# Performance work log

Hardware: AMD Instinct MI355X
Metric: run time of the kernel (lower is better)

The kernel has to match this reference:

```python
import jax, jax.numpy as jnp
import numpy as np
import math

L = 6        # num_layers
H = 16       # nhead
D = 1024     # feature_dim (= d_model, dim_factor=1)
DFF = 1024
IN = 1024    # input_dim
B, T = 16, 512
HD = D // H
EPS = 1e-5


def _get_slopes(n):
    def pow2(n):
        start = 2.0 ** (-2.0 ** (-(math.log2(n) - 3)))
        return [start * (start ** i) for i in range(n)]
    if math.log2(n).is_integer():
        return pow2(n)
    cp2 = 2 ** math.floor(math.log2(n))
    return pow2(cp2) + _get_slopes(2 * cp2)[0::2][: n - cp2]


def _alibi_bias(num_heads, seq_len):
    # init_alibi_biased_mask_future reduces to -slope_h * |i - j|
    slopes = jnp.asarray(_get_slopes(num_heads), dtype=jnp.float32)  # [H]
    idx = jnp.arange(seq_len)
    rel = -jnp.abs(idx[:, None] - idx[None, :]).astype(jnp.float32)  # [T,T]
    return slopes[:, None, None] * rel  # [H,T,T]


def _ln(x, w, b):
    m = jnp.mean(x, axis=-1, keepdims=True)
    v = jnp.mean(jnp.square(x - m), axis=-1, keepdims=True)
    return (x - m) * jax.lax.rsqrt(v + EPS) * w + b


def setup_inputs() -> dict:
    key = jax.random.key(0)
    ks = jax.random.split(key, 16)
    s = 0.02
    return {
        "x": jax.random.normal(ks[0], (B, T, IN), dtype=jnp.float32),
        "bn_w": jax.random.normal(ks[1], (D, IN), dtype=jnp.float32) * s,
        "bn_b": jnp.zeros((D,), jnp.float32),
        "qkv_w": jax.random.normal(ks[2], (L, 3 * D, D), dtype=jnp.float32) * s,
        "qkv_b": jnp.zeros((L, 3 * D), jnp.float32),
        "out_w": jax.random.normal(ks[3], (L, D, D), dtype=jnp.float32) * s,
        "out_b": jnp.zeros((L, D), jnp.float32),
        "ln1_w": jnp.ones((L, D), jnp.float32),
        "ln1_b": jnp.zeros((L, D), jnp.float32),
        "ln2_w": jnp.ones((L, D), jnp.float32),
        "ln2_b": jnp.zeros((L, D), jnp.float32),
        "ff1_w": jax.random.normal(ks[4], (L, DFF, D), dtype=jnp.float32) * s,
        "ff1_b": jnp.zeros((L, DFF), jnp.float32),
        "ff2_w": jax.random.normal(ks[5], (L, D, DFF), dtype=jnp.float32) * s,
        "ff2_b": jnp.zeros((L, D), jnp.float32),
    }


def reference(x, bn_w, bn_b, qkv_w, qkv_b, out_w, out_b,
              ln1_w, ln1_b, ln2_w, ln2_b, ff1_w, ff1_b, ff2_w, ff2_b):
    b, t, _ = x.shape
    bias = _alibi_bias(H, t)  # [H,T,T], same for all batch elements
    h = x @ bn_w.T + bn_b  # bottleneck -> [B,T,D]
    scale = 1.0 / math.sqrt(HD)
    for l in range(L):
        qkv = h @ qkv_w[l].T + qkv_b[l]  # [B,T,3D]
        q, k, v = jnp.split(qkv, 3, axis=-1)
        q = q.reshape(b, t, H, HD)
        k = k.reshape(b, t, H, HD)
        v = v.reshape(b, t, H, HD)
        scores = jnp.einsum('bihd,bjhd->bhij', q, k) * scale + bias[None]
        attn = jax.nn.softmax(scores, axis=-1)
        o = jnp.einsum('bhij,bjhd->bihd', attn, v).reshape(b, t, D)
        o = o @ out_w[l].T + out_b[l]
        h = _ln(h + o, ln1_w[l], ln1_b[l])  # post-norm (PyTorch default)
        f = jax.nn.gelu(h @ ff1_w[l].T + ff1_b[l], approximate=False)
        f = f @ ff2_w[l].T + ff2_b[l]
        h = _ln(h + f, ln2_w[l], ln2_b[l])
    return h
```

## Files before the change

### kernel.cpp

```cpp
#include <hip/hip_runtime.h>
#include <stdint.h>

#define DEV static __device__ __forceinline__

typedef __attribute__((ext_vector_type(8))) uint16_t u16x8;
typedef __attribute__((ext_vector_type(4))) uint16_t u16x4;
typedef __attribute__((ext_vector_type(4))) float    f32x4;
typedef __attribute__((ext_vector_type(8))) __bf16   bf16x8;

typedef __attribute__((address_space(3))) void lds_void;
typedef __attribute__((address_space(1))) void gbl_void;

DEV float bf2f(uint16_t u){
  union { uint32_t i; float f; } v; v.i = ((uint32_t)u) << 16; return v.f;
}
DEV uint16_t f2bf(float f){ return __builtin_bit_cast(uint16_t, (__bf16)f); }
DEV f32x4 mfma16(u16x8 a, u16x8 b, f32x4 c){
  return __builtin_amdgcn_mfma_f32_16x16x32_bf16(
      __builtin_bit_cast(bf16x8, a), __builtin_bit_cast(bf16x8, b), c, 0, 0, 0);
}

__global__ __launch_bounds__(256)
void te_cvt(const float* __restrict__ in, uint16_t* __restrict__ out)
{
  const size_t i = ((size_t)blockIdx.x * 256 + threadIdx.x) * 8;
  f32x4 a = *(const f32x4*)(in + i);
  f32x4 b = *(const f32x4*)(in + i + 4);
  u16x8 o;
#pragma unroll
  for (int e = 0; e < 4; e++) {
    o[e]     = f2bf(a[e]);
    o[e + 4] = f2bf(b[e]);
  }
  *(u16x8*)(out + i) = o;
}

template<int MODE>
__global__ __launch_bounds__(256)
void te_gemm_bb(const uint16_t* __restrict__ A, int lda,
                const uint16_t* __restrict__ W, const float* __restrict__ bias,
                uint16_t* __restrict__ outB, float* __restrict__ outF,
                int M, int N, int K)
{
  __shared__ uint16_t la[128 * 64];
  __shared__ uint16_t lb[128 * 64];
  const int tid = threadIdx.x;
  const int w = tid >> 6, l = tid & 63;
  const int lr = l & 15, lg = l >> 4;
  const int tm = blockIdx.y * 128, tn = blockIdx.x * 128;
  const int srow = l >> 3;
  const int scol = ((l & 7) ^ srow) * 8;
  const int wr = (w >> 1) * 64, wc = (w & 1) * 64;

  f32x4 acc[4][4] = {};

  for (int k0 = 0; k0 < K; k0 += 64) {
#pragma unroll
    for (int c = 0; c < 4; c++) {
      const int rb = (c * 4 + w) * 8;
      const uint16_t* ga = A + (size_t)(tm + rb + srow) * lda + (k0 + scol);
      __builtin_amdgcn_global_load_lds((gbl_void*)(uintptr_t)ga,
                                       (lds_void*)(la + rb * 64), 16, 0, 0);
      const uint16_t* gw = W + (size_t)(tn + rb + srow) * K + (k0 + scol);
      __builtin_amdgcn_global_load_lds((gbl_void*)(uintptr_t)gw,
                                       (lds_void*)(lb + rb * 64), 16, 0, 0);
    }
    __syncthreads();
#pragma unroll
    for (int kk = 0; kk < 2; kk++) {
      u16x8 af[4], bfr[4];
#pragma unroll
      for (int i = 0; i < 4; i++) {
        const int row = wr + i * 16 + lr;
        af[i] = *(const u16x8*)&la[row * 64 + (((kk * 4 + lg) ^ (lr & 7)) << 3)];
      }
#pragma unroll
      for (int j = 0; j < 4; j++) {
        const int row = wc + j * 16 + lr;
        bfr[j] = *(const u16x8*)&lb[row * 64 + (((kk * 4 + lg) ^ (lr & 7)) << 3)];
      }
#pragma unroll
      for (int i = 0; i < 4; i++)
#pragma unroll
        for (int j = 0; j < 4; j++)
          acc[i][j] = mfma16(af[i], bfr[j], acc[i][j]);
    }
    __syncthreads();
  }

  float bv[4];
#pragma unroll
  for (int j = 0; j < 4; j++) bv[j] = bias[tn + wc + j * 16 + lr];
#pragma unroll
  for (int i = 0; i < 4; i++)
#pragma unroll
    for (int j = 0; j < 4; j++)
#pragma unroll
      for (int r = 0; r < 4; r++) {
        const int row = tm + wr + i * 16 + lg * 4 + r;
        const int col = tn + wc + j * 16 + lr;
        float v = acc[i][j][r] + bv[j];
        if (MODE == 2) {
          const float u = 0.7978845608028654f * v * (1.0f + 0.044715f * v * v);
          const float t = 1.0f - 2.0f / (__expf(2.0f * u) + 1.0f);
          v = 0.5f * v * (1.0f + t);
        }
        const size_t idx = (size_t)row * N + col;
        outB[idx] = f2bf(v);
        if (MODE == 1) outF[idx] = v;
      }
}

__global__ __launch_bounds__(256)
void te_attn(uint16_t* __restrict__ qkv)
{
  __shared__ uint16_t kl[64 * 64];
  __shared__ uint16_t vt[64 * 64];
  __shared__ uint16_t pl[4 * 16 * 64];
  const int tid = threadIdx.x;
  const int w = tid >> 6, l = tid & 63;
  const int lr = l & 15, lg = l >> 4;
  const int bh = blockIdx.x;
  const int qt = blockIdx.y;
  const int h  = bh & 15;
  const int b  = bh >> 4;

  u16x8 qf[2];
  {
    const size_t qoff = ((size_t)(b * 512 + qt * 64 + w * 16 + lr)) * 3072 + h * 64 + lg * 8;
    qf[0] = *(const u16x8*)&qkv[qoff];
    qf[1] = *(const u16x8*)&qkv[qoff + 32];
  }
  const float slope = exp2f(-0.5f * (float)(h + 1));
  const float scale = 0.125f;
  const int iBase = qt * 64 + w * 16 + lg * 4;

  float m[4], sd[4];
  f32x4 acc[4] = {};
#pragma unroll
  for (int r = 0; r < 4; r++) { m[r] = -1e30f; sd[r] = 0.0f; }

  for (int jt = 0; jt < 512; jt += 64) {
#pragma unroll
    for (int cc = 0; cc < 2; cc++) {
      const int c = tid + cc * 256;
      const int j = c >> 3, d0 = (c & 7) * 8;
      const size_t rbase = ((size_t)(b * 512 + jt + j)) * 3072 + h * 64 + d0;
      u16x8 kv = *(const u16x8*)&qkv[rbase + 1024];
      *(u16x8*)&kl[j * 64 + (((d0 >> 3) ^ (j & 7)) << 3)] = kv;
      u16x8 vv = *(const u16x8*)&qkv[rbase + 2048];
      const int cV = (((j >> 3) ^ (d0 >> 3)) << 3) + (j & 7);
#pragma unroll
      for (int e = 0; e < 8; e++) vt[(d0 + e) * 64 + cV] = vv[e];
    }
    __syncthreads();

    f32x4 s[4] = {};
#pragma unroll
    for (int kk = 0; kk < 2; kk++) {
#pragma unroll
      for (int n = 0; n < 4; n++) {
        const int row = n * 16 + lr;
        u16x8 kf = *(const u16x8*)&kl[row * 64 + (((kk * 4 + lg) ^ (lr & 7)) << 3)];
        s[n] = mfma16(qf[kk], kf, s[n]);
      }
    }
    float mt[4] = { -1e30f, -1e30f, -1e30f, -1e30f };
#pragma unroll
    for (int n = 0; n < 4; n++)
#pragma unroll
      for (int r = 0; r < 4; r++) {
        const int dj = (iBase + r) - (jt + n * 16 + lr);
        const float v = s[n][r] * scale - slope * fabsf((float)dj);
        s[n][r] = v;
        mt[r] = fmaxf(mt[r], v);
      }
#pragma unroll
    for (int r = 0; r < 4; r++)
#pragma unroll
      for (int msk = 1; msk < 16; msk <<= 1)
        mt[r] = fmaxf(mt[r], __shfl_xor(mt[r], msk, 16));
    float fac[4], rsum[4];
#pragma unroll
    for (int r = 0; r < 4; r++) {
      const float mn = fmaxf(m[r], mt[r]);
      fac[r] = __expf(m[r] - mn);
      m[r] = mn;
      rsum[r] = 0.0f;
    }
#pragma unroll
    for (int n = 0; n < 4; n++)
#pragma unroll
      for (int r = 0; r < 4; r++) {
        const float p = __expf(s[n][r] - m[r]);
        s[n][r] = p;
        rsum[r] += p;
      }
#pragma unroll
    for (int r = 0; r < 4; r++) {
#pragma unroll
      for (int msk = 1; msk < 16; msk <<= 1)
        rsum[r] += __shfl_xor(rsum[r], msk, 16);
      sd[r] = sd[r] * fac[r] + rsum[r];
    }
#pragma unroll
    for (int n = 0; n < 4; n++)
#pragma unroll
      for (int r = 0; r < 4; r++) acc[n][r] *= fac[r];

#pragma unroll
    for (int n = 0; n < 4; n++)
#pragma unroll
      for (int r = 0; r < 4; r++) {
        const int q = lg * 4 + r;
        const int chunk = ((2 * n + (lr >> 3)) ^ (q & 7)) & 7;
        pl[w * 1024 + q * 64 + chunk * 8 + (lr & 7)] = f2bf(s[n][r]);
      }

#pragma unroll
    for (int kk = 0; kk < 2; kk++) {
      u16x8 pf = *(const u16x8*)&pl[w * 1024 + lr * 64 + (((kk * 4 + lg) ^ (lr & 7)) << 3)];
#pragma unroll
      for (int n = 0; n < 4; n++) {
        const int row = n * 16 + lr;
        u16x8 vf = *(const u16x8*)&vt[row * 64 + ((((kk * 4 + lg) ^ (2 * n + (lr >> 3))) & 7) << 3)];
        acc[n] = mfma16(pf, vf, acc[n]);
      }
    }
    __syncthreads();
  }

#pragma unroll
  for (int n = 0; n < 4; n++)
#pragma unroll
    for (int r = 0; r < 4; r++) {
      const int i = iBase + r;
      const int d = h * 64 + n * 16 + lr;
      qkv[((size_t)(b * 512 + i)) * 3072 + d] = f2bf(acc[n][r] / sd[r]);
    }
}

template<int FINAL>
__global__ __launch_bounds__(256)
void te_ln(const float* __restrict__ hres, const uint16_t* __restrict__ delta,
           const float* __restrict__ w, const float* __restrict__ b,
           float* __restrict__ hout, uint16_t* __restrict__ bout)
{
  const int row = blockIdx.x, t = threadIdx.x;
  const size_t base = (size_t)row * 1024 + t * 4;
  f32x4 hv = *(const f32x4*)&hres[base];
  u16x4 dv = *(const u16x4*)&delta[base];
  float x[4];
#pragma unroll
  for (int i = 0; i < 4; i++) x[i] = hv[i] + bf2f(dv[i]);
  float s = x[0] + x[1] + x[2] + x[3];
  float ss = x[0]*x[0] + x[1]*x[1] + x[2]*x[2] + x[3]*x[3];
#pragma unroll
  for (int msk = 32; msk >= 1; msk >>= 1) {
    s  += __shfl_xor(s, msk);
    ss += __shfl_xor(ss, msk);
  }
  __shared__ float rs[4], rq[4];
  const int wv = t >> 6;
  if ((t & 63) == 0) { rs[wv] = s; rq[wv] = ss; }
  __syncthreads();
  s  = rs[0] + rs[1] + rs[2] + rs[3];
  ss = rq[0] + rq[1] + rq[2] + rq[3];
  const float mean = s * (1.0f / 1024.0f);
  const float var  = ss * (1.0f / 1024.0f) - mean * mean;
  const float rstd = rsqrtf(var + 1e-5f);
  f32x4 wv4 = *(const f32x4*)&w[t * 4];
  f32x4 bv4 = *(const f32x4*)&b[t * 4];
  f32x4 yo; u16x4 bo;
#pragma unroll
  for (int i = 0; i < 4; i++) {
    const float y = (x[i] - mean) * rstd * wv4[i] + bv4[i];
    yo[i] = y; bo[i] = f2bf(y);
  }
  *(f32x4*)&hout[base] = yo;
  if (FINAL == 0) *(u16x4*)&bout[base] = bo;
}

extern "C" void kernel_launch(void* const* d_in, const int* in_sizes, int n_in,
                              void* d_out, int out_size, void* d_ws, size_t ws_size,
                              hipStream_t stream)
{
  (void)in_sizes; (void)n_in; (void)out_size; (void)ws_size;
  const float* x     = (const float*)d_in[0];
  const float* bn_w  = (const float*)d_in[1];
  const float* bn_b  = (const float*)d_in[2];
  const float* qkv_w = (const float*)d_in[3];
  const float* qkv_b = (const float*)d_in[4];
  const float* out_w = (const float*)d_in[5];
  const float* out_b = (const float*)d_in[6];
  const float* ln1_w = (const float*)d_in[7];
  const float* ln1_b = (const float*)d_in[8];
  const float* ln2_w = (const float*)d_in[9];
  const float* ln2_b = (const float*)d_in[10];
  const float* ff1_w = (const float*)d_in[11];
  const float* ff1_b = (const float*)d_in[12];
  const float* ff2_w = (const float*)d_in[13];
  const float* ff2_b = (const float*)d_in[14];

  char* ws = (char*)d_ws;
  float*    h_f32   = (float*)ws;
  uint16_t* h_bf    = (uint16_t*)(ws + (32u  << 20));
  uint16_t* qkvb    = (uint16_t*)(ws + (48u  << 20));
  uint16_t* scrA    = (uint16_t*)(ws + (96u  << 20));
  uint16_t* qkvw_bf = (uint16_t*)(ws + (112u << 20));
  uint16_t* ff2w_bf = (uint16_t*)(ws + (148u << 20));
  uint16_t* bnw_bf  = (uint16_t*)(ws + (160u << 20));
  uint16_t* outw_bf = (uint16_t*)d_out;
  uint16_t* ff1w_bf = (uint16_t*)((char*)d_out + (12u << 20));
  float*    outf    = (float*)d_out;

  const int M = 8192;
  dim3 blk(256);

  te_cvt<<<dim3(18874368 / 2048), blk, 0, stream>>>(qkv_w, qkvw_bf);
  te_cvt<<<dim3(6291456  / 2048), blk, 0, stream>>>(out_w, outw_bf);
  te_cvt<<<dim3(6291456  / 2048), blk, 0, stream>>>(ff1_w, ff1w_bf);
  te_cvt<<<dim3(6291456  / 2048), blk, 0, stream>>>(ff2_w, ff2w_bf);
  te_cvt<<<dim3(1048576  / 2048), blk, 0, stream>>>(bn_w,  bnw_bf);
  te_cvt<<<dim3(8388608  / 2048), blk, 0, stream>>>(x,     scrA);

  te_gemm_bb<1><<<dim3(8, 64), blk, 0, stream>>>(scrA, 1024, bnw_bf, bn_b,
                                                 h_bf, h_f32, M, 1024, 1024);

  for (int l = 0; l < 6; l++) {
    te_gemm_bb<0><<<dim3(24, 64), blk, 0, stream>>>(
        h_bf, 1024, qkvw_bf + (size_t)l * 3072 * 1024, qkv_b + l * 3072,
        qkvb, nullptr, M, 3072, 1024);
    te_attn<<<dim3(256, 8), blk, 0, stream>>>(qkvb);
    te_gemm_bb<0><<<dim3(8, 64), blk, 0, stream>>>(
        qkvb, 3072, outw_bf + (size_t)l * 1024 * 1024, out_b + l * 1024,
        scrA, nullptr, M, 1024, 1024);
    te_ln<0><<<dim3(8192), blk, 0, stream>>>(h_f32, scrA, ln1_w + l * 1024, ln1_b + l * 1024,
                                             h_f32, h_bf);
    te_gemm_bb<2><<<dim3(8, 64), blk, 0, stream>>>(
        h_bf, 1024, ff1w_bf + (size_t)l * 1024 * 1024, ff1_b + l * 1024,
        scrA, nullptr, M, 1024, 1024);
    te_gemm_bb<0><<<dim3(8, 64), blk, 0, stream>>>(
        scrA, 1024, ff2w_bf + (size_t)l * 1024 * 1024, ff2_b + l * 1024,
        qkvb, nullptr, M, 1024, 1024);
    if (l == 5) {
      te_ln<1><<<dim3(8192), blk, 0, stream>>>(h_f32, qkvb, ln2_w + l * 1024, ln2_b + l * 1024,
                                               outf, nullptr);
    } else {
      te_ln<0><<<dim3(8192), blk, 0, stream>>>(h_f32, qkvb, ln2_w + l * 1024, ln2_b + l * 1024,
                                               h_f32, h_bf);
    }
  }
}
```

Measured before the change: 1.714 ms.

## Restructure attention: transposed QK, register P reshuffle, K/V prefetch, lazy rescale

The attention kernel now computes S^T (K as the A operand), so each lane owns a single query row. That turns the row-max and row-sum reductions into two cross-lane shuffles instead of four 16-lane butterflies. P is packed to bf16 with v_cvt_pk_bf16 and redistributed through shuffles instead of a round trip through LDS. The next K/V tile is prefetched into registers while the current one is computed, tiles are visited in a rotated order per query tile, and the accumulator rescale is skipped when no row max grows. It also adds s_setprio around the MFMA groups in both GEMM and attention, at the cost of extra shuffles and register pressure.

```diff
diff --git a/kernel.cpp b/kernel.cpp
--- a/kernel.cpp
+++ b/kernel.cpp
@@ -5,6 +5,7 @@
 
 typedef __attribute__((ext_vector_type(8))) uint16_t u16x8;
 typedef __attribute__((ext_vector_type(4))) uint16_t u16x4;
+typedef __attribute__((ext_vector_type(4))) uint32_t u32x4;
 typedef __attribute__((ext_vector_type(4))) float    f32x4;
 typedef __attribute__((ext_vector_type(8))) __bf16   bf16x8;
 
@@ -18,6 +19,11 @@
 DEV f32x4 mfma16(u16x8 a, u16x8 b, f32x4 c){
   return __builtin_amdgcn_mfma_f32_16x16x32_bf16(
       __builtin_bit_cast(bf16x8, a), __builtin_bit_cast(bf16x8, b), c, 0, 0, 0);
+}
+DEV uint32_t cvt_pk_bf16(float lo, float hi){
+  uint32_t r;
+  asm("v_cvt_pk_bf16_f32 %0, %1, %2" : "=v"(r) : "v"(lo), "v"(hi));
+  return r;
 }
 
 __global__ __launch_bounds__(256)
@@ -79,11 +85,13 @@
         const int row = wc + j * 16 + lr;
         bfr[j] = *(const u16x8*)&lb[row * 64 + (((kk * 4 + lg) ^ (lr & 7)) << 3)];
       }
+      __builtin_amdgcn_s_setprio(1);
 #pragma unroll
       for (int i = 0; i < 4; i++)
 #pragma unroll
         for (int j = 0; j < 4; j++)
           acc[i][j] = mfma16(af[i], bfr[j], acc[i][j]);
+      __builtin_amdgcn_s_setprio(0);
     }
     __syncthreads();
   }
@@ -116,127 +124,165 @@
 {
   __shared__ uint16_t kl[64 * 64];
   __shared__ uint16_t vt[64 * 64];
-  __shared__ uint16_t pl[4 * 16 * 64];
   const int tid = threadIdx.x;
   const int w = tid >> 6, l = tid & 63;
   const int lr = l & 15, lg = l >> 4;
-  const int bh = blockIdx.x;
-  const int qt = blockIdx.y;
-  const int h  = bh & 15;
-  const int b  = bh >> 4;
-
+  const int bh = blockIdx.x, qt = blockIdx.y;
+  const int h = bh & 15, b = bh >> 4;
+
+  const int iQ = qt * 64 + w * 16 + lr;
   u16x8 qf[2];
   {
-    const size_t qoff = ((size_t)(b * 512 + qt * 64 + w * 16 + lr)) * 3072 + h * 64 + lg * 8;
+    const size_t qoff = ((size_t)(b * 512 + iQ)) * 3072 + h * 64 + lg * 8;
     qf[0] = *(const u16x8*)&qkv[qoff];
     qf[1] = *(const u16x8*)&qkv[qoff + 32];
   }
-  const float slope = exp2f(-0.5f * (float)(h + 1));
-  const float scale = 0.125f;
-  const int iBase = qt * 64 + w * 16 + lg * 4;
-
-  float m[4], sd[4];
+  const float LOG2E  = 1.4426950408889634f;
+  const float scl2e  = 0.125f * LOG2E;
+  const float slope2e = exp2f(-0.5f * (float)(h + 1)) * LOG2E;
+
+  const int sjb = tid >> 3;
+  const int sd0 = (tid & 7) * 8;
+
+  float mR = -1e30f, sdq = 0.0f;
   f32x4 acc[4] = {};
-#pragma unroll
-  for (int r = 0; r < 4; r++) { m[r] = -1e30f; sd[r] = 0.0f; }
-
-  for (int jt = 0; jt < 512; jt += 64) {
+
+  u16x8 kreg[2], vreg[2];
+  {
+    const int jt0 = (qt & 7) * 64;
 #pragma unroll
     for (int cc = 0; cc < 2; cc++) {
-      const int c = tid + cc * 256;
-      const int j = c >> 3, d0 = (c & 7) * 8;
-      const size_t rbase = ((size_t)(b * 512 + jt + j)) * 3072 + h * 64 + d0;
-      u16x8 kv = *(const u16x8*)&qkv[rbase + 1024];
-      *(u16x8*)&kl[j * 64 + (((d0 >> 3) ^ (j & 7)) << 3)] = kv;
-      u16x8 vv = *(const u16x8*)&qkv[rbase + 2048];
-      const int cV = (((j >> 3) ^ (d0 >> 3)) << 3) + (j & 7);
-#pragma unroll
-      for (int e = 0; e < 8; e++) vt[(d0 + e) * 64 + cV] = vv[e];
+      const int j = sjb + cc * 32;
+      const size_t rbase = ((size_t)(b * 512 + jt0 + j)) * 3072 + h * 64 + sd0;
+      kreg[cc] = *(const u16x8*)&qkv[rbase + 1024];
+      vreg[cc] = *(const u16x8*)&qkv[rbase + 2048];
+    }
+  }
+
+  for (int step = 0; step < 8; step++) {
+    const int jt = ((qt + step) & 7) * 64;
+#pragma unroll
+    for (int cc = 0; cc < 2; cc++) {
+      const int j = sjb + cc * 32;
+      *(u16x8*)&kl[j * 64 + (((sd0 >> 3) ^ (j & 7)) << 3)] = kreg[cc];
+      const int cV = (((j >> 3) ^ (sd0 >> 3)) << 3) + (j & 7);
+#pragma unroll
+      for (int e = 0; e < 8; e++) vt[(sd0 + e) * 64 + cV] = vreg[cc][e];
     }
     __syncthreads();
+    if (step < 7) {
+      const int jtn = ((qt + step + 1) & 7) * 64;
+#pragma unroll
+      for (int cc = 0; cc < 2; cc++) {
+        const int j = sjb + cc * 32;
+        const size_t rbase = ((size_t)(b * 512 + jtn + j)) * 3072 + h * 64 + sd0;
+        kreg[cc] = *(const u16x8*)&qkv[rbase + 1024];
+        vreg[cc] = *(const u16x8*)&qkv[rbase + 2048];
+      }
+    }
 
     f32x4 s[4] = {};
 #pragma unroll
     for (int kk = 0; kk < 2; kk++) {
+      u16x8 kf[4];
 #pragma unroll
       for (int n = 0; n < 4; n++) {
         const int row = n * 16 + lr;
-        u16x8 kf = *(const u16x8*)&kl[row * 64 + (((kk * 4 + lg) ^ (lr & 7)) << 3)];
-        s[n] = mfma16(qf[kk], kf, s[n]);
-      }
-    }
-    float mt[4] = { -1e30f, -1e30f, -1e30f, -1e30f };
+        kf[n] = *(const u16x8*)&kl[row * 64 + (((kk * 4 + lg) ^ (lr & 7)) << 3)];
+      }
+      __builtin_amdgcn_s_setprio(1);
+#pragma unroll
+      for (int n = 0; n < 4; n++)
+        s[n] = mfma16(kf[n], qf[kk], s[n]);
+      __builtin_amdgcn_s_setprio(0);
+    }
+
+    const float f0 = (float)(iQ - jt - lg * 4);
+    float mt = -1e30f;
+#pragma unroll
+    for (int n = 0; n < 4; n++) {
+      const float fj = f0 - (float)(n * 16);
+#pragma unroll
+      for (int r = 0; r < 4; r++) {
+        const float v = fmaf(s[n][r], scl2e, -slope2e * fabsf(fj - (float)r));
+        s[n][r] = v;
+        mt = fmaxf(mt, v);
+      }
+    }
+    mt = fmaxf(mt, __shfl_xor(mt, 16));
+    mt = fmaxf(mt, __shfl_xor(mt, 32));
+
+    if (!__all(mt <= mR)) {
+      const float mN = fmaxf(mR, mt);
+      const float fq = exp2f(mR - mN);
+      mR = mN;
+      sdq *= fq;
+      float fA[4];
+#pragma unroll
+      for (int r = 0; r < 4; r++) fA[r] = __shfl(fq, lg * 4 + r);
+#pragma unroll
+      for (int n = 0; n < 4; n++)
+#pragma unroll
+        for (int r = 0; r < 4; r++) acc[n][r] *= fA[r];
+    }
+
+    float rs = 0.0f;
 #pragma unroll
     for (int n = 0; n < 4; n++)
 #pragma unroll
       for (int r = 0; r < 4; r++) {
-        const int dj = (iBase + r) - (jt + n * 16 + lr);
-        const float v = s[n][r] * scale - slope * fabsf((float)dj);
-        s[n][r] = v;
-        mt[r] = fmaxf(mt[r], v);
-      }
-#pragma unroll
-    for (int r = 0; r < 4; r++)
-#pragma unroll
-      for (int msk = 1; msk < 16; msk <<= 1)
-        mt[r] = fmaxf(mt[r], __shfl_xor(mt[r], msk, 16));
-    float fac[4], rsum[4];
-#pragma unroll
-    for (int r = 0; r < 4; r++) {
-      const float mn = fmaxf(m[r], mt[r]);
-      fac[r] = __expf(m[r] - mn);
-      m[r] = mn;
-      rsum[r] = 0.0f;
-    }
-#pragma unroll
-    for (int n = 0; n < 4; n++)
-#pragma unroll
-      for (int r = 0; r < 4; r++) {
-        const float p = __expf(s[n][r] - m[r]);
+        const float p = exp2f(s[n][r] - mR);
         s[n][r] = p;
-        rsum[r] += p;
-      }
-#pragma unroll
-    for (int r = 0; r < 4; r++) {
-#pragma unroll
-      for (int msk = 1; msk < 16; msk <<= 1)
-        rsum[r] += __shfl_xor(rsum[r], msk, 16);
-      sd[r] = sd[r] * fac[r] + rsum[r];
-    }
-#pragma unroll
-    for (int n = 0; n < 4; n++)
-#pragma unroll
-      for (int r = 0; r < 4; r++) acc[n][r] *= fac[r];
-
-#pragma unroll
-    for (int n = 0; n < 4; n++)
-#pragma unroll
-      for (int r = 0; r < 4; r++) {
-        const int q = lg * 4 + r;
-        const int chunk = ((2 * n + (lr >> 3)) ^ (q & 7)) & 7;
-        pl[w * 1024 + q * 64 + chunk * 8 + (lr & 7)] = f2bf(s[n][r]);
-      }
+        rs += p;
+      }
+    rs += __shfl_xor(rs, 16);
+    rs += __shfl_xor(rs, 32);
+    sdq += rs;
+
+    uint32_t P2[4][2];
+#pragma unroll
+    for (int n = 0; n < 4; n++) {
+      P2[n][0] = cvt_pk_bf16(s[n][0], s[n][1]);
+      P2[n][1] = cvt_pk_bf16(s[n][2], s[n][3]);
+    }
 
 #pragma unroll
     for (int kk = 0; kk < 2; kk++) {
-      u16x8 pf = *(const u16x8*)&pl[w * 1024 + lr * 64 + (((kk * 4 + lg) ^ (lr & 7)) << 3)];
+      uint32_t pw[4];
+#pragma unroll
+      for (int t = 0; t < 4; t++) {
+        const int srcLane = lr + 16 * ((lg & 1) * 2 + (t >> 1));
+        const uint32_t xa = __shfl(P2[2 * kk + 0][t & 1], srcLane);
+        const uint32_t xb = __shfl(P2[2 * kk + 1][t & 1], srcLane);
+        pw[t] = (lg >> 1) ? xb : xa;
+      }
+      u32x4 pv4 = { pw[0], pw[1], pw[2], pw[3] };
+      u16x8 pf = __builtin_bit_cast(u16x8, pv4);
+      u16x8 vf[4];
 #pragma unroll
       for (int n = 0; n < 4; n++) {
         const int row = n * 16 + lr;
-        u16x8 vf = *(const u16x8*)&vt[row * 64 + ((((kk * 4 + lg) ^ (2 * n + (lr >> 3))) & 7) << 3)];
-        acc[n] = mfma16(pf, vf, acc[n]);
-      }
+        vf[n] = *(const u16x8*)&vt[row * 64 + ((((kk * 4 + lg) ^ (2 * n + (lr >> 3))) & 7) << 3)];
+      }
+      __builtin_amdgcn_s_setprio(1);
+#pragma unroll
+      for (int n = 0; n < 4; n++)
+        acc[n] = mfma16(pf, vf[n], acc[n]);
+      __builtin_amdgcn_s_setprio(0);
     }
     __syncthreads();
   }
 
+  float sdA[4];
+#pragma unroll
+  for (int r = 0; r < 4; r++) sdA[r] = 1.0f / __shfl(sdq, lg * 4 + r);
 #pragma unroll
   for (int n = 0; n < 4; n++)
 #pragma unroll
     for (int r = 0; r < 4; r++) {
-      const int i = iBase + r;
+      const int i = qt * 64 + w * 16 + lg * 4 + r;
       const int d = h * 64 + n * 16 + lr;
-      qkv[((size_t)(b * 512 + i)) * 3072 + d] = f2bf(acc[n][r] / sd[r]);
+      qkv[((size_t)(b * 512 + i)) * 3072 + d] = f2bf(acc[n][r] * sdA[r]);
     }
 }
 
```

Measured after the change: 1.567 ms. 1.09x faster.
